# Kernel optimization log

Hardware: AMD Instinct MI355X
Metric: run time of the kernel (lower is better)

## Reference

```python
import jax, jax.numpy as jnp
import numpy as np

H = 384
W = 384
C_X = 64       # channels of x (== out_channels)
C_PTX = 64     # channels of ptx
C_IN = C_X + C_PTX  # Linear in_channels = 128
C_OUT = 64
N_TGT = 120000  # number of target pixels (CSR segments)
DEG = 8         # points per target pixel
N_PTS = N_TGT * DEG


def setup_inputs() -> dict:
    key = jax.random.key(0)
    k1, k2, k3, k4 = jax.random.split(key, 4)
    x = jax.random.normal(k1, (1, C_X, H, W), jnp.float32)
    ptx = jax.random.normal(k2, (N_PTS, C_PTX), jnp.float32)
    # CSR row pointer over points per target pixel (monotone, ends at N_PTS)
    point_key = jnp.arange(N_TGT + 1, dtype=jnp.int32) * DEG
    # unique target-pixel indices into H*W
    pixel_tgt_idx = jnp.arange(N_TGT, dtype=jnp.int32)
    sm_w = jax.random.normal(k3, (C_IN, 1), jnp.float32) * 0.05
    sm_b = jnp.zeros((1,), jnp.float32)
    fo_w = jax.random.normal(k4, (C_IN, C_OUT), jnp.float32) * 0.05
    fo_b = jnp.zeros((C_OUT,), jnp.float32)
    return {"x": x, "ptx": ptx, "sm_w": sm_w, "sm_b": sm_b,
            "fo_w": fo_w, "fo_b": fo_b, "point_key": point_key,
            "pixel_tgt_idx": pixel_tgt_idx, "bs": 1, "height": H, "width": W}


def reference(x, ptx, sm_w, sm_b, fo_w, fo_b, point_key, pixel_tgt_idx, bs, height, width):
    # segment id per point from CSR rowptr (static total length for jit)
    seg = jnp.repeat(jnp.arange(N_TGT, dtype=jnp.int32), jnp.diff(point_key),
                     total_repeat_length=N_PTS)
    # pixel features gathered to target pixels, then CSR-gathered to points
    feat_px = x.transpose(0, 2, 3, 1).reshape(height * width, C_X)[pixel_tgt_idx]
    feat = jnp.concatenate([ptx, feat_px[seg]], axis=1)  # [N_PTS, C_IN]
    # _net_forward: identity (base class)
    # segment softmax over points within each pixel group
    logits = feat @ sm_w + sm_b  # [N_PTS, 1]
    m = jax.ops.segment_max(logits, seg, num_segments=N_TGT)
    e = jnp.exp(logits - m[seg])
    s = jax.ops.segment_sum(e, seg, num_segments=N_TGT)
    weight = e / (s[seg] + 1e-16)
    # feat_out projection replaces ptx
    ptx_out = feat @ fo_w + fo_b  # [N_PTS, C_OUT]
    agg = jax.ops.segment_sum(weight * ptx_out, seg, num_segments=N_TGT)  # [N_TGT, C_OUT]
    # list_to_map: scatter aggregated features back to image grid + mask
    flat = jnp.zeros((height * width, C_OUT), x.dtype).at[pixel_tgt_idx].set(agg)
    mask = jnp.zeros((height * width, 1), x.dtype).at[pixel_tgt_idx].set(1.0)
    fmap = flat.reshape(1, height, width, C_OUT).transpose(0, 3, 1, 2)
    mmap = mask.reshape(1, height, width, 1).transpose(0, 3, 1, 2)
    x_out = jnp.where(mmap > 0, fmap, x)
    return x_out, ptx_out
```

## Files before the change

kernel.cpp:

```cpp
#include <hip/hip_runtime.h>
#include <hip/hip_bf16.h>
#include <math.h>

typedef __attribute__((ext_vector_type(8))) short short8v;
typedef __attribute__((ext_vector_type(4))) float float4v;

#define TB 128

__device__ __forceinline__ short f2bf(float f) {
    __hip_bfloat16 h = __float2bfloat16(f);
    short s; __builtin_memcpy(&s, &h, sizeof(short));
    return s;
}
__device__ __forceinline__ float4v mfma_bf16(short8v a, short8v b, float4v c) {
    return __builtin_amdgcn_mfma_f32_16x16x32_bf16(a, b, c, 0, 0, 0);
}

__global__ __launch_bounds__(256)
void copy_x_kernel(const float4* __restrict__ x, float4* __restrict__ out, int n4) {
    int i = blockIdx.x * blockDim.x + threadIdx.x;
    if (i < n4) out[i] = x[i];
}

__global__ __launch_bounds__(256, 3)
void fused_kernel(const float* __restrict__ x,
                  const float* __restrict__ ptx,
                  const float* __restrict__ sm_w,
                  const float* __restrict__ fo_w,
                  const float* __restrict__ fo_b,
                  const int* __restrict__ point_key,
                  const int* __restrict__ pixel_tgt_idx,
                  float* __restrict__ xout,
                  float* __restrict__ ptx_out,
                  int n_tgt, int n_pts, int hw)
{
    __shared__ __align__(16) char sraw[2 * 128 * 72 * 2];
    unsigned short (*fpx)[72] = (unsigned short (*)[72])sraw;
    unsigned short (*wT)[72]  = (unsigned short (*)[72])(sraw + 128 * 72 * 2);
    float (*agg)[68]          = (float (*)[68])sraw;
    __shared__ int pix_s[TB], r0_s[TB], deg_s[TB];

    const int tid  = threadIdx.x;
    const int lane = tid & 63;
    const int w    = tid >> 6;
    const int lo16 = lane & 15;
    const int g    = lane >> 4;
    const int t0   = blockIdx.x * TB;

    if (tid < TB) {
        int t = t0 + tid;
        bool v = t < n_tgt;
        int r0 = v ? point_key[t] : 0;
        int d  = v ? (point_key[t + 1] - r0) : 0;
        pix_s[tid] = v ? pixel_tgt_idx[t] : 0;
        r0_s[tid]  = r0;
        deg_s[tid] = d > 8 ? 8 : d;
    }
    {
        const float4* fw4 = (const float4*)fo_w;
        #pragma unroll
        for (int i = 0; i < 8; ++i) {
            int idx4 = i * 256 + tid;
            float4 v = fw4[idx4];
            int flat = idx4 * 4;
            int k = flat >> 6, c = flat & 63;
            int wrow0 = (k & 64) + c;
            int col = k & 63;
            wT[wrow0 + 0][col] = (unsigned short)f2bf(v.x);
            wT[wrow0 + 1][col] = (unsigned short)f2bf(v.y);
            wT[wrow0 + 2][col] = (unsigned short)f2bf(v.z);
            wT[wrow0 + 3][col] = (unsigned short)f2bf(v.w);
        }
    }
    __syncthreads();

    {
        const int tgt = tid >> 1, half = tid & 1;
        const int pix = pix_s[tgt];
        const float* xp = x + (size_t)(half * 32) * hw + pix;
        #pragma unroll
        for (int ch = 0; ch < 4; ++ch) {
            short8v pk;
            #pragma unroll
            for (int j = 0; j < 8; ++j)
                pk[j] = f2bf(xp[(size_t)(ch * 8 + j) * hw]);
            *(short8v*)&fpx[tgt][half * 32 + ch * 8] = pk;
        }
    }
    short8v b1[5][2];
    #pragma unroll
    for (int ct = 0; ct < 4; ++ct)
        #pragma unroll
        for (int kh = 0; kh < 2; ++kh)
            b1[ct][kh] = *(const short8v*)&wT[ct * 16 + lo16][kh * 32 + g * 8];
    #pragma unroll
    for (int kh = 0; kh < 2; ++kh) {
        short8v bb;
        #pragma unroll
        for (int j = 0; j < 8; ++j)
            bb[j] = (lo16 == 0) ? f2bf(sm_w[kh * 32 + g * 8 + j]) : (short)0;
        b1[4][kh] = bb;
    }
    float fb[4];
    #pragma unroll
    for (int ct = 0; ct < 4; ++ct) fb[ct] = fo_b[ct * 16 + lo16];
    __syncthreads();

    const int tw0 = w * 32;
    float4v qreg[2][4];
    {
        short8v a2[2][2];
        #pragma unroll
        for (int mq = 0; mq < 2; ++mq)
            #pragma unroll
            for (int kh = 0; kh < 2; ++kh)
                a2[mq][kh] = *(const short8v*)&fpx[tw0 + mq * 16 + lo16][kh * 32 + g * 8];
        #pragma unroll
        for (int ct = 0; ct < 4; ++ct) {
            short8v b20 = *(const short8v*)&wT[64 + ct * 16 + lo16][g * 8];
            short8v b21 = *(const short8v*)&wT[64 + ct * 16 + lo16][32 + g * 8];
            #pragma unroll
            for (int mq = 0; mq < 2; ++mq) {
                float4v z = {0.f, 0.f, 0.f, 0.f};
                z = mfma_bf16(a2[mq][0], b20, z);
                z = mfma_bf16(a2[mq][1], b21, z);
                #pragma unroll
                for (int r = 0; r < 4; ++r) qreg[mq][ct][r] = z[r] + fb[ct];
            }
        }
    }
    __syncthreads();

    #pragma unroll
    for (int mq = 0; mq < 2; ++mq)
    for (int mtl2 = 0; mtl2 < 4; ++mtl2) {
        #pragma unroll
        for (int u = 0; u < 2; ++u) {
            const int mt  = mq * 8 + mtl2 * 2 + u;
            const int tlA = tw0 + mt * 2 + (lo16 >> 3);
            int pg = r0_s[tlA] + (lo16 & 7);
            if (pg >= n_pts) pg = n_pts - 1;
            const float* prow = ptx + (size_t)pg * 64 + g * 8;
            short8v a[2];
            #pragma unroll
            for (int kh = 0; kh < 2; ++kh) {
                float4 f0 = *(const float4*)(prow + kh * 32);
                float4 f1 = *(const float4*)(prow + kh * 32 + 4);
                short8v aa;
                aa[0] = f2bf(f0.x); aa[1] = f2bf(f0.y); aa[2] = f2bf(f0.z); aa[3] = f2bf(f0.w);
                aa[4] = f2bf(f1.x); aa[5] = f2bf(f1.y); aa[6] = f2bf(f1.z); aa[7] = f2bf(f1.w);
                a[kh] = aa;
            }
            float4v c[5];
            #pragma unroll
            for (int ct = 0; ct < 5; ++ct) {
                float4v z = {0.f, 0.f, 0.f, 0.f};
                z = mfma_bf16(a[0], b1[ct][0], z);
                c[ct] = mfma_bf16(a[1], b1[ct][1], z);
            }

            const int tE   = tw0 + mt * 2 + (g >> 1);
            const int degE = deg_s[tE];
            const int r0E  = r0_s[tE];
            float lgt[4];
            #pragma unroll
            for (int r = 0; r < 4; ++r) {
                float v = __shfl(c[4][r], lane & 48);
                lgt[r] = (((g & 1) * 4 + r) < degE) ? v : -3.4e38f;
            }
            float m4 = fmaxf(fmaxf(lgt[0], lgt[1]), fmaxf(lgt[2], lgt[3]));
            float m8 = fmaxf(m4, __shfl_xor(m4, 16));
            float wgt[4], wsum = 0.f;
            #pragma unroll
            for (int r = 0; r < 4; ++r) {
                int pE = (g & 1) * 4 + r;
                wgt[r] = (pE < degE) ? __expf(lgt[r] - m8) : 0.0f;
                wsum += wgt[r];
            }
            wsum += __shfl_xor(wsum, 16);
            const float inv = 1.0f / (wsum + 1e-16f);

            const int srcLane = mtl2 * 16 + lo16;
            #pragma unroll
            for (int ct = 0; ct < 4; ++ct) {
                float q0 = __shfl(qreg[mq][ct][2 * u],     srcLane);
                float q1 = __shfl(qreg[mq][ct][2 * u + 1], srcLane);
                float qv = (g & 2) ? q1 : q0;
                int col = ct * 16 + lo16;
                float ap = 0.f;
                #pragma unroll
                for (int r = 0; r < 4; ++r) {
                    float po = c[ct][r] + qv;
                    int pE = (g & 1) * 4 + r;
                    if (pE < degE)
                        ptx_out[(size_t)(r0E + pE) * 64 + col] = po;
                    ap = fmaf(wgt[r] * inv, po, ap);
                }
                ap += __shfl_xor(ap, 16);
                if (!(lane & 16)) agg[tE][col] = ap;
            }
        }
    }
    __syncthreads();

    {
        const int tgt = tid >> 1, half = tid & 1;
        if (t0 + tgt < n_tgt) {
            const int pix = pix_s[tgt];
            float* xp = xout + (size_t)(half * 32) * hw + pix;
            #pragma unroll
            for (int ch = 0; ch < 8; ++ch) {
                float4 v = *(const float4*)&agg[tgt][half * 32 + ch * 4];
                xp[(size_t)(ch * 4 + 0) * hw] = v.x;
                xp[(size_t)(ch * 4 + 1) * hw] = v.y;
                xp[(size_t)(ch * 4 + 2) * hw] = v.z;
                xp[(size_t)(ch * 4 + 3) * hw] = v.w;
            }
        }
    }
}

extern "C" void kernel_launch(void* const* d_in, const int* in_sizes, int n_in,
                              void* d_out, int out_size, void* d_ws, size_t ws_size,
                              hipStream_t stream) {
    const float* x             = (const float*)d_in[0];
    const float* ptx           = (const float*)d_in[1];
    const float* sm_w          = (const float*)d_in[2];
    const float* fo_w          = (const float*)d_in[4];
    const float* fo_b          = (const float*)d_in[5];
    const int*   point_key     = (const int*)d_in[6];
    const int*   pixel_tgt_idx = (const int*)d_in[7];

    const int x_elems = in_sizes[0];
    const int hw      = x_elems / 64;
    const int n_tgt   = in_sizes[7];
    const int n_pts   = in_sizes[1] / 64;

    float* xout    = (float*)d_out;
    float* ptx_out = xout + (size_t)x_elems;

    const int n4 = x_elems / 4;
    copy_x_kernel<<<(n4 + 255) / 256, 256, 0, stream>>>(
        (const float4*)x, (float4*)xout, n4);

    const int blocks = (n_tgt + TB - 1) / TB;
    fused_kernel<<<blocks, 256, 0, stream>>>(
        x, ptx, sm_w, fo_w, fo_b, point_key, pixel_tgt_idx,
        xout, ptx_out, n_tgt, n_pts, hw);
}
```

Measured before the change: 155.1 us.

## Halve targets per block, prefetch ptx rows, stage q in LDS

Cuts the targets per block from 128 to 64 so each wave handles 16 targets, and raises the occupancy hint to 4 blocks per CU. The per-target q projection now goes through LDS instead of lane shuffles. ptx rows are software-prefetched one tile ahead, and the fo_w global loads are issued before the index setup. The aim is to hide gather latency with more resident waves and overlapped loads. The cost is twice as many blocks, so the fo_w transpose and conversion into LDS is repeated more often.

```diff
diff --git a/kernel.cpp b/kernel.cpp
--- a/kernel.cpp
+++ b/kernel.cpp
@@ -5,7 +5,7 @@
 typedef __attribute__((ext_vector_type(8))) short short8v;
 typedef __attribute__((ext_vector_type(4))) float float4v;
 
-#define TB 128
+#define TB 64
 
 __device__ __forceinline__ short f2bf(float f) {
     __hip_bfloat16 h = __float2bfloat16(f);
@@ -22,7 +22,7 @@
     if (i < n4) out[i] = x[i];
 }
 
-__global__ __launch_bounds__(256, 3)
+__global__ __launch_bounds__(256, 4)
 void fused_kernel(const float* __restrict__ x,
                   const float* __restrict__ ptx,
                   const float* __restrict__ sm_w,
@@ -34,10 +34,11 @@
                   float* __restrict__ ptx_out,
                   int n_tgt, int n_pts, int hw)
 {
-    __shared__ __align__(16) char sraw[2 * 128 * 72 * 2];
+    __shared__ __align__(16) char sraw[34816];
     unsigned short (*fpx)[72] = (unsigned short (*)[72])sraw;
-    unsigned short (*wT)[72]  = (unsigned short (*)[72])(sraw + 128 * 72 * 2);
-    float (*agg)[68]          = (float (*)[68])sraw;
+    unsigned short (*wT)[72]  = (unsigned short (*)[72])(sraw + 9216);
+    float (*q_lds)[68]        = (float (*)[68])sraw;
+    float (*agg)[68]          = (float (*)[68])(sraw + 17408);
     __shared__ int pix_s[TB], r0_s[TB], deg_s[TB];
 
     const int tid  = threadIdx.x;
@@ -46,7 +47,14 @@
     const int lo16 = lane & 15;
     const int g    = lane >> 4;
     const int t0   = blockIdx.x * TB;
-
+    const int tw0  = w * 16;
+
+    float4 wv[8];
+    {
+        const float4* fw4 = (const float4*)fo_w;
+        #pragma unroll
+        for (int i = 0; i < 8; ++i) wv[i] = fw4[i * 256 + tid];
+    }
     if (tid < TB) {
         int t = t0 + tid;
         bool v = t < n_tgt;
@@ -56,37 +64,37 @@
         r0_s[tid]  = r0;
         deg_s[tid] = d > 8 ? 8 : d;
     }
-    {
-        const float4* fw4 = (const float4*)fo_w;
-        #pragma unroll
-        for (int i = 0; i < 8; ++i) {
-            int idx4 = i * 256 + tid;
-            float4 v = fw4[idx4];
-            int flat = idx4 * 4;
-            int k = flat >> 6, c = flat & 63;
-            int wrow0 = (k & 64) + c;
-            int col = k & 63;
-            wT[wrow0 + 0][col] = (unsigned short)f2bf(v.x);
-            wT[wrow0 + 1][col] = (unsigned short)f2bf(v.y);
-            wT[wrow0 + 2][col] = (unsigned short)f2bf(v.z);
-            wT[wrow0 + 3][col] = (unsigned short)f2bf(v.w);
-        }
-    }
-    __syncthreads();
-
-    {
-        const int tgt = tid >> 1, half = tid & 1;
+    float fb[4];
+    #pragma unroll
+    for (int ct = 0; ct < 4; ++ct) fb[ct] = fo_b[ct * 16 + lo16];
+
+    #pragma unroll
+    for (int i = 0; i < 8; ++i) {
+        int flat = (i * 256 + tid) * 4;
+        int k = flat >> 6, c = flat & 63;
+        int wrow0 = (k & 64) + c;
+        int col = k & 63;
+        wT[wrow0 + 0][col] = (unsigned short)f2bf(wv[i].x);
+        wT[wrow0 + 1][col] = (unsigned short)f2bf(wv[i].y);
+        wT[wrow0 + 2][col] = (unsigned short)f2bf(wv[i].z);
+        wT[wrow0 + 3][col] = (unsigned short)f2bf(wv[i].w);
+    }
+    __syncthreads();
+
+    {
+        const int tgt = tid >> 2, q4 = tid & 3;
         const int pix = pix_s[tgt];
-        const float* xp = x + (size_t)(half * 32) * hw + pix;
-        #pragma unroll
-        for (int ch = 0; ch < 4; ++ch) {
+        const float* xp = x + (size_t)(q4 * 16) * hw + pix;
+        #pragma unroll
+        for (int hhalf = 0; hhalf < 2; ++hhalf) {
             short8v pk;
             #pragma unroll
             for (int j = 0; j < 8; ++j)
-                pk[j] = f2bf(xp[(size_t)(ch * 8 + j) * hw]);
-            *(short8v*)&fpx[tgt][half * 32 + ch * 8] = pk;
-        }
-    }
+                pk[j] = f2bf(xp[(size_t)(hhalf * 8 + j) * hw]);
+            *(short8v*)&fpx[tgt][q4 * 16 + hhalf * 8] = pk;
+        }
+    }
+
     short8v b1[5][2];
     #pragma unroll
     for (int ct = 0; ct < 4; ++ct)
@@ -101,120 +109,111 @@
             bb[j] = (lo16 == 0) ? f2bf(sm_w[kh * 32 + g * 8 + j]) : (short)0;
         b1[4][kh] = bb;
     }
-    float fb[4];
-    #pragma unroll
-    for (int ct = 0; ct < 4; ++ct) fb[ct] = fo_b[ct * 16 + lo16];
-    __syncthreads();
-
-    const int tw0 = w * 32;
-    float4v qreg[2][4];
-    {
-        short8v a2[2][2];
-        #pragma unroll
-        for (int mq = 0; mq < 2; ++mq)
-            #pragma unroll
-            for (int kh = 0; kh < 2; ++kh)
-                a2[mq][kh] = *(const short8v*)&fpx[tw0 + mq * 16 + lo16][kh * 32 + g * 8];
+    __syncthreads();
+
+    float4v qv4[4];
+    {
+        short8v a20 = *(const short8v*)&fpx[tw0 + lo16][g * 8];
+        short8v a21 = *(const short8v*)&fpx[tw0 + lo16][32 + g * 8];
         #pragma unroll
         for (int ct = 0; ct < 4; ++ct) {
             short8v b20 = *(const short8v*)&wT[64 + ct * 16 + lo16][g * 8];
             short8v b21 = *(const short8v*)&wT[64 + ct * 16 + lo16][32 + g * 8];
-            #pragma unroll
-            for (int mq = 0; mq < 2; ++mq) {
-                float4v z = {0.f, 0.f, 0.f, 0.f};
-                z = mfma_bf16(a2[mq][0], b20, z);
-                z = mfma_bf16(a2[mq][1], b21, z);
-                #pragma unroll
-                for (int r = 0; r < 4; ++r) qreg[mq][ct][r] = z[r] + fb[ct];
-            }
-        }
-    }
-    __syncthreads();
-
-    #pragma unroll
-    for (int mq = 0; mq < 2; ++mq)
-    for (int mtl2 = 0; mtl2 < 4; ++mtl2) {
-        #pragma unroll
-        for (int u = 0; u < 2; ++u) {
-            const int mt  = mq * 8 + mtl2 * 2 + u;
-            const int tlA = tw0 + mt * 2 + (lo16 >> 3);
-            int pg = r0_s[tlA] + (lo16 & 7);
-            if (pg >= n_pts) pg = n_pts - 1;
-            const float* prow = ptx + (size_t)pg * 64 + g * 8;
-            short8v a[2];
-            #pragma unroll
-            for (int kh = 0; kh < 2; ++kh) {
-                float4 f0 = *(const float4*)(prow + kh * 32);
-                float4 f1 = *(const float4*)(prow + kh * 32 + 4);
-                short8v aa;
-                aa[0] = f2bf(f0.x); aa[1] = f2bf(f0.y); aa[2] = f2bf(f0.z); aa[3] = f2bf(f0.w);
-                aa[4] = f2bf(f1.x); aa[5] = f2bf(f1.y); aa[6] = f2bf(f1.z); aa[7] = f2bf(f1.w);
-                a[kh] = aa;
-            }
-            float4v c[5];
-            #pragma unroll
-            for (int ct = 0; ct < 5; ++ct) {
-                float4v z = {0.f, 0.f, 0.f, 0.f};
-                z = mfma_bf16(a[0], b1[ct][0], z);
-                c[ct] = mfma_bf16(a[1], b1[ct][1], z);
-            }
-
-            const int tE   = tw0 + mt * 2 + (g >> 1);
-            const int degE = deg_s[tE];
-            const int r0E  = r0_s[tE];
-            float lgt[4];
+            float4v z = {0.f, 0.f, 0.f, 0.f};
+            z = mfma_bf16(a20, b20, z);
+            qv4[ct] = mfma_bf16(a21, b21, z);
+        }
+    }
+    __syncthreads();
+    #pragma unroll
+    for (int ct = 0; ct < 4; ++ct)
+        #pragma unroll
+        for (int r = 0; r < 4; ++r)
+            q_lds[tw0 + g * 4 + r][ct * 16 + lo16] = qv4[ct][r] + fb[ct];
+
+    float4 buf0, buf1, buf2, buf3;
+    auto LOADA = [&](int mt) {
+        const int tlA = tw0 + mt * 2 + (lo16 >> 3);
+        int pg = r0_s[tlA] + (lo16 & 7);
+        if (pg >= n_pts) pg = n_pts - 1;
+        const float* prow = ptx + (size_t)pg * 64 + g * 8;
+        buf0 = *(const float4*)(prow);
+        buf1 = *(const float4*)(prow + 4);
+        buf2 = *(const float4*)(prow + 32);
+        buf3 = *(const float4*)(prow + 36);
+    };
+    LOADA(0);
+    #pragma unroll
+    for (int mt = 0; mt < 8; ++mt) {
+        const float4 c0 = buf0, c1 = buf1, c2 = buf2, c3 = buf3;
+        if (mt < 7) LOADA(mt + 1);
+
+        short8v a0, a1;
+        a0[0] = f2bf(c0.x); a0[1] = f2bf(c0.y); a0[2] = f2bf(c0.z); a0[3] = f2bf(c0.w);
+        a0[4] = f2bf(c1.x); a0[5] = f2bf(c1.y); a0[6] = f2bf(c1.z); a0[7] = f2bf(c1.w);
+        a1[0] = f2bf(c2.x); a1[1] = f2bf(c2.y); a1[2] = f2bf(c2.z); a1[3] = f2bf(c2.w);
+        a1[4] = f2bf(c3.x); a1[5] = f2bf(c3.y); a1[6] = f2bf(c3.z); a1[7] = f2bf(c3.w);
+
+        float4v c[5];
+        #pragma unroll
+        for (int ct = 0; ct < 5; ++ct) {
+            float4v z = {0.f, 0.f, 0.f, 0.f};
+            z = mfma_bf16(a0, b1[ct][0], z);
+            c[ct] = mfma_bf16(a1, b1[ct][1], z);
+        }
+
+        const int tE   = tw0 + mt * 2 + (g >> 1);
+        const int degE = deg_s[tE];
+        const int r0E  = r0_s[tE];
+        float lgt[4];
+        #pragma unroll
+        for (int r = 0; r < 4; ++r) {
+            float v = __shfl(c[4][r], lane & 48);
+            lgt[r] = (((g & 1) * 4 + r) < degE) ? v : -3.4e38f;
+        }
+        float m4 = fmaxf(fmaxf(lgt[0], lgt[1]), fmaxf(lgt[2], lgt[3]));
+        float m8 = fmaxf(m4, __shfl_xor(m4, 16));
+        float wgt[4], wsum = 0.f;
+        #pragma unroll
+        for (int r = 0; r < 4; ++r) {
+            int pE = (g & 1) * 4 + r;
+            wgt[r] = (pE < degE) ? __expf(lgt[r] - m8) : 0.0f;
+            wsum += wgt[r];
+        }
+        wsum += __shfl_xor(wsum, 16);
+        const float inv = 1.0f / (wsum + 1e-16f);
+
+        #pragma unroll
+        for (int ct = 0; ct < 4; ++ct) {
+            const int col = ct * 16 + lo16;
+            const float qv = q_lds[tE][col];
+            float ap = 0.f;
             #pragma unroll
             for (int r = 0; r < 4; ++r) {
-                float v = __shfl(c[4][r], lane & 48);
-                lgt[r] = (((g & 1) * 4 + r) < degE) ? v : -3.4e38f;
+                float po = c[ct][r] + qv;
+                int pE = (g & 1) * 4 + r;
+                if (pE < degE)
+                    ptx_out[(size_t)(r0E + pE) * 64 + col] = po;
+                ap = fmaf(wgt[r] * inv, po, ap);
             }
-            float m4 = fmaxf(fmaxf(lgt[0], lgt[1]), fmaxf(lgt[2], lgt[3]));
-            float m8 = fmaxf(m4, __shfl_xor(m4, 16));
-            float wgt[4], wsum = 0.f;
-            #pragma unroll
-            for (int r = 0; r < 4; ++r) {
-                int pE = (g & 1) * 4 + r;
-                wgt[r] = (pE < degE) ? __expf(lgt[r] - m8) : 0.0f;
-                wsum += wgt[r];
-            }
-            wsum += __shfl_xor(wsum, 16);
-            const float inv = 1.0f / (wsum + 1e-16f);
-
-            const int srcLane = mtl2 * 16 + lo16;
-            #pragma unroll
-            for (int ct = 0; ct < 4; ++ct) {
-                float q0 = __shfl(qreg[mq][ct][2 * u],     srcLane);
-                float q1 = __shfl(qreg[mq][ct][2 * u + 1], srcLane);
-                float qv = (g & 2) ? q1 : q0;
-                int col = ct * 16 + lo16;
-                float ap = 0.f;
-                #pragma unroll
-                for (int r = 0; r < 4; ++r) {
-                    float po = c[ct][r] + qv;
-                    int pE = (g & 1) * 4 + r;
-                    if (pE < degE)
-                        ptx_out[(size_t)(r0E + pE) * 64 + col] = po;
-                    ap = fmaf(wgt[r] * inv, po, ap);
-                }
-                ap += __shfl_xor(ap, 16);
-                if (!(lane & 16)) agg[tE][col] = ap;
-            }
-        }
-    }
-    __syncthreads();
-
-    {
-        const int tgt = tid >> 1, half = tid & 1;
+            ap += __shfl_xor(ap, 16);
+            if (!(lane & 16)) agg[tE][col] = ap;
+        }
+    }
+    __syncthreads();
+
+    {
+        const int tgt = tid >> 2, q4 = tid & 3;
         if (t0 + tgt < n_tgt) {
             const int pix = pix_s[tgt];
-            float* xp = xout + (size_t)(half * 32) * hw + pix;
+            float* xp = xout + (size_t)(q4 * 16) * hw + pix;
             #pragma unroll
-            for (int ch = 0; ch < 8; ++ch) {
-                float4 v = *(const float4*)&agg[tgt][half * 32 + ch * 4];
-                xp[(size_t)(ch * 4 + 0) * hw] = v.x;
-                xp[(size_t)(ch * 4 + 1) * hw] = v.y;
-                xp[(size_t)(ch * 4 + 2) * hw] = v.z;
-                xp[(size_t)(ch * 4 + 3) * hw] = v.w;
+            for (int u = 0; u < 4; ++u) {
+                float4 v = *(const float4*)&agg[tgt][q4 * 16 + u * 4];
+                xp[(size_t)(u * 4 + 0) * hw] = v.x;
+                xp[(size_t)(u * 4 + 1) * hw] = v.y;
+                xp[(size_t)(u * 4 + 2) * hw] = v.z;
+                xp[(size_t)(u * 4 + 3) * hw] = v.w;
             }
         }
     }
```

Result: faster. 143.0 us (-7.8%).
